# Kernel optimization log

Measured on AMD Instinct MI355X. Metric: run time of the kernel, lower is better.

## Reference

```python
import jax, jax.numpy as jnp
import numpy as np

B, L, D_MODEL = 2, 2048, 512
EXPAND = 2
ED = EXPAND * D_MODEL          # d_inner = 1024
N = 16                          # d_state
D_CONV = 4
DT_RANK = (D_MODEL + N - 1) // N  # 32
D_FF = 1024
EPS = 1e-5


def _mamba_params(key, pre):
    ks = jax.random.split(key, 6)
    s = 0.02
    p = {}
    p[pre + 'in_w'] = jax.random.normal(ks[0], (D_MODEL, 2 * ED), jnp.float32) * s
    p[pre + 'conv_w'] = jax.random.normal(ks[1], (ED, 1, D_CONV), jnp.float32) * s
    p[pre + 'conv_b'] = jnp.zeros((ED,), jnp.float32)
    p[pre + 'xproj_w'] = jax.random.normal(ks[2], (ED, DT_RANK + 2 * N), jnp.float32) * s
    p[pre + 'dt_w'] = jax.random.normal(ks[3], (DT_RANK, ED), jnp.float32) * s
    p[pre + 'dt_b'] = jax.random.normal(ks[4], (ED,), jnp.float32) * s
    # S4D-real init: A_log = log(1..N) per channel
    p[pre + 'A_log'] = jnp.log(jnp.broadcast_to(jnp.arange(1, N + 1, dtype=jnp.float32), (ED, N)))
    p[pre + 'D'] = jnp.ones((ED,), jnp.float32)
    p[pre + 'out_w'] = jax.random.normal(ks[5], (ED, D_MODEL), jnp.float32) * s
    return p


def setup_inputs() -> dict:
    key = jax.random.key(0)
    k_x, k_f, k_b, k_ffn = jax.random.split(key, 4)
    inp = {'x': jax.random.normal(k_x, (B, L, D_MODEL), jnp.float32)}
    inp.update(_mamba_params(k_f, 'f_'))
    inp.update(_mamba_params(k_b, 'b_'))
    inp['norm1_g'] = jnp.ones((D_MODEL,), jnp.float32)
    inp['norm1_b'] = jnp.zeros((D_MODEL,), jnp.float32)
    inp['norm2_g'] = jnp.ones((D_MODEL,), jnp.float32)
    inp['norm2_b'] = jnp.zeros((D_MODEL,), jnp.float32)
    k1, k2 = jax.random.split(k_ffn)
    inp['ffn_w1'] = jax.random.normal(k1, (D_MODEL, D_FF), jnp.float32) * 0.02
    inp['ffn_b1'] = jnp.zeros((D_FF,), jnp.float32)
    inp['ffn_w2'] = jax.random.normal(k2, (D_FF, D_MODEL), jnp.float32) * 0.02
    inp['ffn_b2'] = jnp.zeros((D_MODEL,), jnp.float32)
    return inp


def _selective_scan(x, delta, A, Bm, C, Dp):
    # x, delta: (B,L,ED); A: (ED,N); Bm, C: (B,L,N); Dp: (ED,)
    def step(h, inp):
        x_t, d_t, B_t, C_t = inp  # (B,ED),(B,ED),(B,N),(B,N)
        dA = jnp.exp(d_t[..., None] * A)                      # (B,ED,N)
        dBx = (d_t * x_t)[..., None] * B_t[:, None, :]        # (B,ED,N)
        h = dA * h + dBx
        y = jnp.einsum('ben,bn->be', h, C_t)
        return h, y

    h0 = jnp.zeros((x.shape[0], ED, N), x.dtype)
    xs = (x.transpose(1, 0, 2), delta.transpose(1, 0, 2),
          Bm.transpose(1, 0, 2), C.transpose(1, 0, 2))
    _, ys = jax.lax.scan(step, h0, xs)
    return ys.transpose(1, 0, 2) + x * Dp


def _mamba(x, in_w, conv_w, conv_b, xproj_w, dt_w, dt_b, A_log, Dp, out_w):
    xz = x @ in_w                                  # (B,L,2*ED)
    xs, z = jnp.split(xz, 2, axis=-1)
    # depthwise causal conv over time
    xc = jax.lax.conv_general_dilated(
        xs.transpose(0, 2, 1), conv_w, (1,), [(D_CONV - 1, 0)],
        dimension_numbers=('NCH', 'OIH', 'NCH'), feature_group_count=ED)
    xc = jax.nn.silu(xc.transpose(0, 2, 1) + conv_b)          # (B,L,ED)
    dbl = xc @ xproj_w                                        # (B,L,DT_RANK+2N)
    dt = dbl[..., :DT_RANK]
    Bm = dbl[..., DT_RANK:DT_RANK + N]
    C = dbl[..., DT_RANK + N:]
    delta = jax.nn.softplus(dt @ dt_w + dt_b)                 # (B,L,ED)
    A = -jnp.exp(A_log)
    y = _selective_scan(xc, delta, A, Bm, C, Dp)
    y = y * jax.nn.silu(z)
    return y @ out_w


def _layernorm(h, g, b):
    mu = jnp.mean(h, axis=-1, keepdims=True)
    var = jnp.var(h, axis=-1, keepdims=True)
    return (h - mu) * jax.lax.rsqrt(var + EPS) * g + b


def _ffn(h, w1, b1, w2, b2):
    return jnp.maximum(h @ w1 + b1, 0.0) @ w2 + b2


def reference(x,
              f_in_w, f_conv_w, f_conv_b, f_xproj_w, f_dt_w, f_dt_b, f_A_log, f_D, f_out_w,
              b_in_w, b_conv_w, b_conv_b, b_xproj_w, b_dt_w, b_dt_b, b_A_log, b_D, b_out_w,
              norm1_g, norm1_b, norm2_g, norm2_b,
              ffn_w1, ffn_b1, ffn_w2, ffn_b2):
    mf = _mamba(x, f_in_w, f_conv_w, f_conv_b, f_xproj_w, f_dt_w, f_dt_b, f_A_log, f_D, f_out_w)
    mf = _layernorm(mf, norm1_g, norm1_b)
    out_f = _ffn(mf, ffn_w1, ffn_b1, ffn_w2, ffn_b2) + mf
    # NOTE: original code computes norm2 but then uses the UN-normalized
    # backward output (variable shadowing bug); we replicate that faithfully.
    mb = _mamba(jnp.flip(x, axis=1), b_in_w, b_conv_w, b_conv_b, b_xproj_w,
                b_dt_w, b_dt_b, b_A_log, b_D, b_out_w)
    out_b = _ffn(mb, ffn_w1, ffn_b1, ffn_w2, ffn_b2) + mb
    return out_f + out_b
```

## Files before the change

### kernel.cpp

```cpp
#include <hip/hip_runtime.h>
#include <hip/hip_bf16.h>
#include <math.h>


#define BD 2
#define LD 2048
#define DMODEL 512
#define EDIM 1024
#define NST 16
#define DTR 32
#define DFF 1024
#define MROWS (BD*LD)

typedef __hip_bfloat16 bf16;
typedef __bf16 bf16x8 __attribute__((ext_vector_type(8)));
typedef float  f32x4  __attribute__((ext_vector_type(4)));

__device__ __forceinline__ float sig_(float x) { return 1.f / (1.f + __expf(-x)); }

__global__ __launch_bounds__(256)
void prep_k(const float* __restrict__ x, bf16* __restrict__ xbf,
            const float* __restrict__ inw_f, const float* __restrict__ inw_b,
            bf16* __restrict__ inwT,
            const float* __restrict__ outw_f, const float* __restrict__ outw_b,
            bf16* __restrict__ outwT,
            const float* __restrict__ fw1, bf16* __restrict__ fw1T,
            const float* __restrict__ fw2, bf16* __restrict__ fw2T)
{
    const int bid = blockIdx.x, tid = threadIdx.x;
    if (bid < 2048) {
        size_t i = (size_t)bid * 1024 + tid * 4;
        float4 v = *(const float4*)(x + i);
        bf16* o = xbf + i;
        o[0] = __float2bfloat16(v.x); o[1] = __float2bfloat16(v.y);
        o[2] = __float2bfloat16(v.z); o[3] = __float2bfloat16(v.w);
        return;
    }
    const float* W; bf16* WT; int R, C, cx, ry;
    if (bid < 4096) {
        int d = (bid - 2048) >> 10, t = (bid - 2048) & 1023;
        W = d ? inw_b : inw_f; WT = inwT + (size_t)d * 2048 * 512;
        R = 512; C = 2048; cx = t & 63; ry = t >> 6;
    } else if (bid < 5120) {
        int d = (bid - 4096) >> 9, t = (bid - 4096) & 511;
        W = d ? outw_b : outw_f; WT = outwT + (size_t)d * 512 * 1024;
        R = 1024; C = 512; cx = t & 15; ry = t >> 4;
    } else if (bid < 5632) {
        int t = bid - 5120; W = fw1; WT = fw1T; R = 512; C = 1024;
        cx = t & 31; ry = t >> 5;
    } else {
        int t = bid - 5632; W = fw2; WT = fw2T; R = 1024; C = 512;
        cx = t & 15; ry = t >> 4;
    }
    __shared__ float tt[32][33];
    const int c0 = cx * 32, r0 = ry * 32;
    const int col = tid & 31, rr = tid >> 5;
#pragma unroll
    for (int p = 0; p < 4; ++p)
        tt[p * 8 + rr][col] = W[(size_t)(r0 + p * 8 + rr) * C + c0 + col];
    __syncthreads();
#pragma unroll
    for (int p = 0; p < 4; ++p)
        WT[(size_t)(c0 + p * 8 + rr) * R + r0 + col] =
            __float2bfloat16(tt[col][p * 8 + rr]);
}

template<int BM, int BN, int MODE, bool FLIPD1>
__global__ __launch_bounds__(256)
void bgemm2_k(const bf16* __restrict__ A, size_t Astr, int lda,
              const bf16* __restrict__ BT, size_t Bstr,
              const float* __restrict__ bias,
              bf16* __restrict__ Cb, size_t Cstr, int ldc,
              const bf16* __restrict__ mp, size_t mpStr,
              float* __restrict__ outp,
              int M, int N, int K, int zoff)
{
    constexpr int FRm = BM / 32, FRn = BN / 32;
    __shared__ __align__(16) bf16 As[BM][40];
    __shared__ __align__(16) bf16 Bs[BN][40];
    const int tid = threadIdx.x;
    const int dir = blockIdx.z + zoff;
    const bool flip = FLIPD1 && (dir == 1);
    const bf16* Ad = A + (size_t)dir * Astr;
    const bf16* Bd = BT + (size_t)dir * Bstr;
    bf16* Cd = Cb ? Cb + (size_t)dir * Cstr : nullptr;
    const bf16* mpd = mp ? mp + (size_t)dir * mpStr : nullptr;
    const int bm = blockIdx.y * BM, bn = blockIdx.x * BN;
    const int wave = tid >> 6, lane = tid & 63;
    const int wm = (wave >> 1) * (BM / 2), wn = (wave & 1) * (BN / 2);
    const int lm = lane & 15, lq = lane >> 4;
    f32x4 acc[FRm][FRn] = {};

    for (int k0 = 0; k0 < K; k0 += 32) {
#pragma unroll
        for (int p = 0; p < BM / 64; ++p) {
            int row = p * 64 + (tid >> 2), col = (tid & 3) * 8;
            int gm = bm + row;
            if (flip) gm = (gm & ~(LD - 1)) + (LD - 1 - (gm & (LD - 1)));
            *(bf16x8*)&As[row][col] =
                *(const bf16x8*)(Ad + (size_t)gm * lda + k0 + col);
        }
#pragma unroll
        for (int p = 0; p < BN / 64; ++p) {
            int row = p * 64 + (tid >> 2), col = (tid & 3) * 8;
            *(bf16x8*)&Bs[row][col] =
                *(const bf16x8*)(Bd + (size_t)(bn + row) * K + k0 + col);
        }
        __syncthreads();

        bf16x8 af[FRm], bfr[FRn];
#pragma unroll
        for (int i = 0; i < FRm; ++i)
            af[i] = *(const bf16x8*)&As[wm + 16 * i + lm][lq * 8];
#pragma unroll
        for (int j = 0; j < FRn; ++j)
            bfr[j] = *(const bf16x8*)&Bs[wn + 16 * j + lm][lq * 8];
#pragma unroll
        for (int i = 0; i < FRm; ++i)
#pragma unroll
            for (int j = 0; j < FRn; ++j)
                acc[i][j] = __builtin_amdgcn_mfma_f32_16x16x32_bf16(
                    af[i], bfr[j], acc[i][j], 0, 0, 0);
        __syncthreads();
    }

#pragma unroll
    for (int i = 0; i < FRm; ++i) {
#pragma unroll
        for (int j = 0; j < FRn; ++j) {
            int col = bn + wn + 16 * j + lm;
            float bv = (MODE >= 2) ? bias[col] : 0.f;
#pragma unroll
            for (int r = 0; r < 4; ++r) {
                int row = bm + wm + 16 * i + lq * 4 + r;
                float v = acc[i][j][r] + bv;
                size_t idx = (size_t)row * ldc + col;
                if (MODE == 0)      Cd[idx] = __float2bfloat16(v);
                else if (MODE == 2) Cd[idx] = __float2bfloat16(fmaxf(v, 0.f));
                else if (MODE == 3) outp[idx] = v + __bfloat162float(mpd[idx]);
                else                outp[idx] += v + __bfloat162float(mpd[idx]);
            }
        }
    }
}

__global__ __launch_bounds__(256)
void zgate_k(const bf16* __restrict__ xbf, const bf16* __restrict__ inwT,
             const bf16* __restrict__ y2t_all, bf16* __restrict__ yrow_all)
{
    __shared__ __align__(16) bf16 As[64][40];
    __shared__ __align__(16) bf16 Bs[128][40];
    __shared__ __bf16 sy[64][130];
    const int tid = threadIdx.x;
    const int dir = blockIdx.z;
    const bf16* Bd = inwT + (size_t)dir * (2048 * 512) + (size_t)1024 * 512;
    const bf16* y2t = y2t_all + (size_t)dir * ((size_t)MROWS * EDIM);
    bf16* yrow = yrow_all + (size_t)dir * ((size_t)MROWS * EDIM);
    const int bm = blockIdx.y * 64, bn = blockIdx.x * 128;
    const int wave = tid >> 6, lane = tid & 63;
    const int wm = (wave >> 1) * 32, wn = (wave & 1) * 64;
    const int lm = lane & 15, lq = lane >> 4;
    f32x4 acc[2][4] = {};

    for (int k0 = 0; k0 < 512; k0 += 32) {
        {
            int row = tid >> 2, col = (tid & 3) * 8;
            int gm = bm + row;
            if (dir == 1) gm = (gm & ~(LD - 1)) + (LD - 1 - (gm & (LD - 1)));
            *(bf16x8*)&As[row][col] =
                *(const bf16x8*)(xbf + (size_t)gm * 512 + k0 + col);
        }
#pragma unroll
        for (int p = 0; p < 2; ++p) {
            int row = p * 64 + (tid >> 2), col = (tid & 3) * 8;
            *(bf16x8*)&Bs[row][col] =
                *(const bf16x8*)(Bd + (size_t)(bn + row) * 512 + k0 + col);
        }
        __syncthreads();
        bf16x8 af[2], bfr[4];
#pragma unroll
        for (int i = 0; i < 2; ++i)
            af[i] = *(const bf16x8*)&As[wm + 16 * i + lm][lq * 8];
#pragma unroll
        for (int j = 0; j < 4; ++j)
            bfr[j] = *(const bf16x8*)&Bs[wn + 16 * j + lm][lq * 8];
#pragma unroll
        for (int i = 0; i < 2; ++i)
#pragma unroll
            for (int j = 0; j < 4; ++j)
                acc[i][j] = __builtin_amdgcn_mfma_f32_16x16x32_bf16(
                    af[i], bfr[j], acc[i][j], 0, 0, 0);
        __syncthreads();
    }

    {
        const int b = bm >> 11, l0 = bm & (LD - 1);
        int e = tid >> 1, lh = (tid & 1) * 32;
        const bf16* yp = y2t + ((size_t)b * EDIM + bn + e) * LD + l0 + lh;
#pragma unroll
        for (int i = 0; i < 4; ++i) {
            bf16x8 v = *(const bf16x8*)(yp + i * 8);
#pragma unroll
            for (int j = 0; j < 8; ++j) sy[lh + i * 8 + j][e] = v[j];
        }
    }
    __syncthreads();
#pragma unroll
    for (int i = 0; i < 2; ++i) {
#pragma unroll
        for (int j = 0; j < 4; ++j) {
            int col = bn + wn + 16 * j + lm;
#pragma unroll
            for (int r = 0; r < 4; ++r) {
                int row = bm + wm + 16 * i + lq * 4 + r;
                float z = acc[i][j][r];
                float g = z * sig_(z);
                float y = (float)sy[(row - bm)][col - bn];
                yrow[(size_t)row * EDIM + col] = __float2bfloat16(g * y);
            }
        }
    }
}

__global__ __launch_bounds__(256)
void conv2_k(const bf16* __restrict__ xs2,
             const float* __restrict__ cw_f, const float* __restrict__ cb_f,
             const float* __restrict__ cw_b, const float* __restrict__ cb_b,
             bf16* __restrict__ xct2)
{
    __shared__ float sxs[67][64];
    __shared__ float sout[64][65];
    const int tid = threadIdx.x;
    const int dir = blockIdx.z;
    const bf16* xs = xs2 + (size_t)dir * ((size_t)MROWS * EDIM);
    const float* w  = dir ? cw_b : cw_f;
    const float* cb = dir ? cb_b : cb_f;
    bf16* xct = xct2 + (size_t)dir * ((size_t)MROWS * EDIM);
    const int e0 = blockIdx.x * 64;
    const int bl0 = blockIdx.y * 64;
    const int lloc0 = bl0 & (LD - 1);
    const int b = bl0 >> 11;
    {
        int row4 = tid >> 6, col = tid & 63;
#pragma unroll
        for (int i = 0; i < 17; ++i) {
            int hr = i * 4 + row4;
            if (hr < 67) {
                int lr = lloc0 + hr - 3;
                sxs[hr][col] = (lr >= 0)
                    ? __bfloat162float(xs[(size_t)(bl0 + hr - 3) * EDIM + e0 + col]) : 0.f;
            }
        }
    }
    __syncthreads();
    {
        int lr4 = tid >> 6, e = tid & 63;
        float w0 = w[(e0 + e) * 4 + 0], w1 = w[(e0 + e) * 4 + 1];
        float w2 = w[(e0 + e) * 4 + 2], w3 = w[(e0 + e) * 4 + 3];
        float cbv = cb[e0 + e];
#pragma unroll
        for (int i = 0; i < 16; ++i) {
            int lr = i * 4 + lr4;
            float acc = cbv;
            acc = fmaf(sxs[lr + 0][e], w0, acc);
            acc = fmaf(sxs[lr + 1][e], w1, acc);
            acc = fmaf(sxs[lr + 2][e], w2, acc);
            acc = fmaf(sxs[lr + 3][e], w3, acc);
            sout[e][lr] = acc * sig_(acc);
        }
    }
    __syncthreads();
    {
        int er4 = tid >> 6, l = tid & 63;
#pragma unroll
        for (int i = 0; i < 16; ++i) {
            int er = i * 4 + er4;
            xct[((size_t)b * EDIM + e0 + er) * LD + lloc0 + l] =
                __float2bfloat16(sout[er][l]);
        }
    }
}

__global__ __launch_bounds__(256)
void g2_k(const bf16* __restrict__ xct2, const float* __restrict__ xp_f,
          const float* __restrict__ xp_b, float* __restrict__ dblt2)
{
    __shared__ __align__(16) float As[32][18];
    __shared__ __align__(16) float Bs[32][66];
    const int tid = threadIdx.x;
    const int dir = blockIdx.y;
    const bf16* xct = xct2 + (size_t)dir * ((size_t)MROWS * EDIM);
    const float* xproj = dir ? xp_b : xp_f;
    float* dblt = dblt2 + (size_t)dir * (2 * 64 * LD);
    const int r0 = blockIdx.x * 16;
    const int bB = r0 >> 11, l0 = r0 & (LD - 1);
    const int row = tid >> 4, col4 = (tid & 15) * 4;
    float acc[4] = {};

    for (int k0 = 0; k0 < EDIM; k0 += 32) {
        {
            int k = tid >> 3, ls = (tid & 7) * 2;
            const bf16* p = xct + ((size_t)bB * EDIM + k0 + k) * LD + l0 + ls;
            As[k][ls] = __bfloat162float(p[0]);
            As[k][ls + 1] = __bfloat162float(p[1]);
        }
        {
            int k = tid >> 3, ns = (tid & 7) * 8;
            const float* p = xproj + (size_t)(k0 + k) * 64 + ns;
            float4 v0 = *(const float4*)p, v1 = *(const float4*)(p + 4);
            float* d = &Bs[k][ns];
            d[0]=v0.x; d[1]=v0.y; d[2]=v0.z; d[3]=v0.w;
            d[4]=v1.x; d[5]=v1.y; d[6]=v1.z; d[7]=v1.w;
        }
        __syncthreads();
#pragma unroll
        for (int kk = 0; kk < 32; ++kk) {
            float a = As[kk][row];
            float4 b4 = *(const float4*)&Bs[kk][col4];
            acc[0] = fmaf(a, b4.x, acc[0]);
            acc[1] = fmaf(a, b4.y, acc[1]);
            acc[2] = fmaf(a, b4.z, acc[2]);
            acc[3] = fmaf(a, b4.w, acc[3]);
        }
        __syncthreads();
    }
#pragma unroll
    for (int j = 0; j < 4; ++j)
        dblt[((size_t)bB * 64 + col4 + j) * LD + l0 + row] = acc[j];
}

__global__ __launch_bounds__(256)
void g3_k(const float* __restrict__ dblt2,
          const float* __restrict__ dtw_f, const float* __restrict__ dtb_f,
          const float* __restrict__ dtw_b, const float* __restrict__ dtb_b,
          bf16* __restrict__ dltt2)
{
    __shared__ __align__(16) float As[16][68];
    __shared__ __align__(16) float Bs[16][68];
    const int tid = threadIdx.x;
    const int dir = blockIdx.z;
    const float* Ap = dblt2 + (size_t)dir * (2 * 64 * LD);
    const float* Bw = dir ? dtw_b : dtw_f;
    const float* bias = dir ? dtb_b : dtb_f;
    bf16* Ct = dltt2 + (size_t)dir * ((size_t)MROWS * EDIM);
    const int bm = blockIdx.y * 64;
    const int bn = blockIdx.x * 64;
    const int bB = bm >> 11, l0 = bm & (LD - 1);
    const int tx = tid & 15, ty = tid >> 4;
    float acc[4][4] = {};

    for (int k0 = 0; k0 < DTR; k0 += 16) {
#pragma unroll
        for (int i = 0; i < 4; ++i) {
            int k = i * 4 + (tid >> 6), ll = tid & 63;
            As[k][ll] = Ap[((size_t)bB * 64 + k0 + k) * LD + l0 + ll];
        }
#pragma unroll
        for (int i = 0; i < 4; ++i) {
            int idx = tid + 256 * i;
            int nl = idx & 63, kl = idx >> 6;
            Bs[kl][nl] = Bw[(size_t)(k0 + kl) * EDIM + bn + nl];
        }
        __syncthreads();
#pragma unroll
        for (int kk = 0; kk < 16; ++kk) {
            float4 av = *(const float4*)&As[kk][ty * 4];
            float4 bv = *(const float4*)&Bs[kk][tx * 4];
            float a[4] = {av.x, av.y, av.z, av.w};
            float b[4] = {bv.x, bv.y, bv.z, bv.w};
#pragma unroll
            for (int i = 0; i < 4; ++i)
#pragma unroll
                for (int j = 0; j < 4; ++j)
                    acc[i][j] = fmaf(a[i], b[j], acc[i][j]);
        }
        __syncthreads();
    }
#pragma unroll
    for (int i = 0; i < 4; ++i) {
        int r = bm + ty * 4 + i;
#pragma unroll
        for (int j = 0; j < 4; ++j) {
            int c = bn + tx * 4 + j;
            float v = acc[i][j] + bias[c];
            v = (v > 20.f) ? v : log1pf(__expf(v));
            Ct[((size_t)(r >> 11) * EDIM + c) * LD + (r & (LD - 1))] =
                __float2bfloat16(v);
        }
    }
}

__global__ __launch_bounds__(256)
void scan6_k(bf16* __restrict__ xct2, const bf16* __restrict__ dltt2,
             const float* __restrict__ dblt2,
             const float* __restrict__ alog_f, const float* __restrict__ alog_b,
             const float* __restrict__ dp_f, const float* __restrict__ dp_b)
{
    __shared__ float sA[NST];
    __shared__ float sWp[NST][4];
    __shared__ float sWs[NST][4];
    const int gid = blockIdx.x;
    const int dir = gid >> 11;
    const int bb  = (gid >> 10) & 1;
    const int e   = gid & (EDIM - 1);
    const float* A_log = dir ? alog_b : alog_f;
    const float* Dp    = dir ? dp_b   : dp_f;
    bf16* xct = xct2 + (size_t)dir * ((size_t)MROWS * EDIM);
    const bf16* dltt = dltt2 + (size_t)dir * ((size_t)MROWS * EDIM);
    const float* bt = dblt2 + (size_t)dir * (2 * 64 * LD) + (size_t)bb * 64 * LD;
    const int tid = threadIdx.x;
    const int wave = tid >> 6, lane = tid & 63;
    const size_t baset = ((size_t)bb * EDIM + e) * LD;
    const int l0 = tid * 8;

    if (tid < NST) sA[tid] = -__expf(A_log[e * NST + tid]);

    float xv[8], dv[8], dx[8];
    {
        bf16x8 xr = *(const bf16x8*)(xct + baset + l0);
        bf16x8 dr = *(const bf16x8*)(dltt + baset + l0);
#pragma unroll
        for (int j = 0; j < 8; ++j) { xv[j] = (float)xr[j]; dv[j] = (float)dr[j]; }
    }
#pragma unroll
    for (int j = 0; j < 8; ++j) dx[j] = dv[j] * xv[j];
    __syncthreads();

    float y[8] = {};
    for (int n = 0; n < NST; ++n) {
        const float An = sA[n];
        const float* Bp = bt + (size_t)(DTR + n) * LD + l0;
        const float* Cp = bt + (size_t)(DTR + NST + n) * LD + l0;
        float4 b0 = *(const float4*)Bp, b1 = *(const float4*)(Bp + 4);
        float4 c0 = *(const float4*)Cp, c1 = *(const float4*)(Cp + 4);
        float Br[8] = {b0.x,b0.y,b0.z,b0.w, b1.x,b1.y,b1.z,b1.w};
        float Cr[8] = {c0.x,c0.y,c0.z,c0.w, c1.x,c1.y,c1.z,c1.w};

        float S[8], P[8];
        float h = 0.f, pr = 1.f;
#pragma unroll
        for (int l = 0; l < 8; ++l) {
            float a = __expf(dv[l] * An);
            pr *= a;
            h = fmaf(a, h, dx[l] * Br[l]);
            P[l] = pr; S[l] = h;
        }

        float p = pr, s = h;
#pragma unroll
        for (int d = 1; d < 64; d <<= 1) {
            float pp = __shfl_up(p, d, 64);
            float sp = __shfl_up(s, d, 64);
            if (lane >= d) { s = fmaf(sp, p, s); p *= pp; }
        }
        if (lane == 63) { sWp[n][wave] = p; sWs[n][wave] = s; }
        __syncthreads();
        float Hoff = 0.f;
#pragma unroll
        for (int w = 0; w < 3; ++w)
            if (w < wave) Hoff = fmaf(sWp[n][w], Hoff, sWs[n][w]);
        float pprev = __shfl_up(p, 1, 64);
        float sprev = __shfl_up(s, 1, 64);
        float H = (lane == 0) ? Hoff : fmaf(pprev, Hoff, sprev);

#pragma unroll
        for (int l = 0; l < 8; ++l)
            y[l] = fmaf(Cr[l], fmaf(P[l], H, S[l]), y[l]);
    }

    const float Dv = Dp[e];
    bf16x8 o;
#pragma unroll
    for (int l = 0; l < 8; ++l) o[l] = (__bf16)fmaf(xv[l], Dv, y[l]);
    *(bf16x8*)(xct + baset + l0) = o;
}

__global__ __launch_bounds__(256)
void ln_k(bf16* __restrict__ m, const float* __restrict__ gg,
          const float* __restrict__ bb)
{
    int row = (blockIdx.x * 256 + threadIdx.x) >> 6;
    int lane = threadIdx.x & 63;
    bf16* r = m + (size_t)row * DMODEL;
    float v[8], s = 0.f, s2 = 0.f;
#pragma unroll
    for (int i = 0; i < 8; ++i) {
        v[i] = __bfloat162float(r[lane + 64 * i]);
        s += v[i]; s2 = fmaf(v[i], v[i], s2);
    }
#pragma unroll
    for (int off = 32; off >= 1; off >>= 1) {
        s  += __shfl_xor(s, off, 64);
        s2 += __shfl_xor(s2, off, 64);
    }
    float mu = s * (1.f / DMODEL);
    float var = s2 * (1.f / DMODEL) - mu * mu;
    float inv = rsqrtf(var + 1e-5f);
#pragma unroll
    for (int i = 0; i < 8; ++i)
        r[lane + 64 * i] = __float2bfloat16(
            (v[i] - mu) * inv * gg[lane + 64 * i] + bb[lane + 64 * i]);
}

__global__ void sentinel_k(float* __restrict__ o)
{
    int i = blockIdx.x * 256 + threadIdx.x;
    o[i] = 100.0f;
}

extern "C" void kernel_launch(void* const* d_in, const int* in_sizes, int n_in,
                              void* d_out, int out_size, void* d_ws, size_t ws_size,
                              hipStream_t stream)
{
    const float* x    = (const float*)d_in[0];
    const float* n1g  = (const float*)d_in[19];
    const float* n1b  = (const float*)d_in[20];
    const float* fw1  = (const float*)d_in[23];
    const float* fb1  = (const float*)d_in[24];
    const float* fw2  = (const float*)d_in[25];
    const float* fb2  = (const float*)d_in[26];
    float* out = (float*)d_out;

    const size_t MiB = 1024 * 1024;
    const size_t SZ_DM = (size_t)MROWS * DMODEL;
    if (ws_size < 46 * MiB) {
        sentinel_k<<<dim3(SZ_DM / 256), dim3(256), 0, stream>>>(out);
        return;
    }

    char* base = (char*)d_ws;
    bf16* fw1T  = (bf16*)base;
    bf16* fw2T  = (bf16*)(base + 1 * MiB);
    bf16* outwT = (bf16*)(base + 2 * MiB);
    bf16* inwT  = (bf16*)(base + 4 * MiB);
    bf16* xbf   = (bf16*)(base + 8 * MiB);
    char* RA    = base + 12 * MiB;
    bf16* xs2   = (bf16*)RA;
    bf16* dltt2 = (bf16*)RA;
    bf16* yrow2 = (bf16*)RA;
    bf16* ffh2  = (bf16*)RA;
    char* RB    = base + 28 * MiB;
    bf16* xct2  = (bf16*)RB;
    bf16* mbf2  = (bf16*)RB;
    float* dblt2 = (float*)(base + 44 * MiB);

    const float* inw_f  = (const float*)d_in[1];
    const float* cw_f   = (const float*)d_in[2];
    const float* cb_f   = (const float*)d_in[3];
    const float* xp_f   = (const float*)d_in[4];
    const float* dtw_f  = (const float*)d_in[5];
    const float* dtb_f  = (const float*)d_in[6];
    const float* alog_f = (const float*)d_in[7];
    const float* dp_f   = (const float*)d_in[8];
    const float* outw_f = (const float*)d_in[9];
    const float* inw_b  = (const float*)d_in[10];
    const float* cw_b   = (const float*)d_in[11];
    const float* cb_b   = (const float*)d_in[12];
    const float* xp_b   = (const float*)d_in[13];
    const float* dtw_b  = (const float*)d_in[14];
    const float* dtb_b  = (const float*)d_in[15];
    const float* alog_b = (const float*)d_in[16];
    const float* dp_b   = (const float*)d_in[17];
    const float* outw_b = (const float*)d_in[18];

    dim3 blk(256);
    const size_t U = (size_t)MROWS * EDIM;

    prep_k<<<dim3(6144), blk, 0, stream>>>(x, xbf, inw_f, inw_b, inwT,
                                           outw_f, outw_b, outwT,
                                           fw1, fw1T, fw2, fw2T);
    bgemm2_k<64, 128, 0, true><<<dim3(8, 64, 2), blk, 0, stream>>>(
        xbf, 0, DMODEL, inwT, (size_t)2048 * 512, nullptr,
        xs2, U, EDIM, nullptr, 0, nullptr, MROWS, EDIM, DMODEL, 0);
    conv2_k<<<dim3(16, 64, 2), blk, 0, stream>>>(xs2, cw_f, cb_f, cw_b, cb_b, xct2);
    g2_k<<<dim3(256, 2), blk, 0, stream>>>(xct2, xp_f, xp_b, dblt2);
    g3_k<<<dim3(16, 64, 2), blk, 0, stream>>>(dblt2, dtw_f, dtb_f, dtw_b, dtb_b, dltt2);
    scan6_k<<<dim3(4096), blk, 0, stream>>>(xct2, dltt2, dblt2,
                                            alog_f, alog_b, dp_f, dp_b);
    zgate_k<<<dim3(8, 64, 2), blk, 0, stream>>>(xbf, inwT, xct2, yrow2);
    bgemm2_k<64, 64, 0, false><<<dim3(8, 64, 2), blk, 0, stream>>>(
        yrow2, U, EDIM, outwT, (size_t)512 * 1024, nullptr,
        mbf2, SZ_DM, DMODEL, nullptr, 0, nullptr, MROWS, DMODEL, EDIM, 0);
    ln_k<<<dim3(MROWS / 4), blk, 0, stream>>>(mbf2, n1g, n1b);
    bgemm2_k<64, 128, 2, false><<<dim3(8, 64, 2), blk, 0, stream>>>(
        mbf2, SZ_DM, DMODEL, fw1T, 0, fb1,
        ffh2, U, DFF, nullptr, 0, nullptr, MROWS, DFF, DMODEL, 0);
    bgemm2_k<64, 64, 3, false><<<dim3(8, 64, 1), blk, 0, stream>>>(
        ffh2, U, DFF, fw2T, 0, fb2,
        nullptr, 0, DMODEL, mbf2, SZ_DM, out, MROWS, DMODEL, DFF, 0);
    bgemm2_k<64, 64, 4, false><<<dim3(8, 64, 1), blk, 0, stream>>>(
        ffh2, U, DFF, fw2T, 0, fb2,
        nullptr, 0, DMODEL, mbf2, SZ_DM, out, MROWS, DMODEL, DFF, 1);
}
```

Measured before the change: 426.9 us.

## Use direct global-to-LDS loads, larger GEMM tiles, merged FFN2 and faster scan exps

GEMM staging now uses global_load_lds builtins with unpadded 128-row tiles. The two FFN second-layer GEMMs (forward and backward) become one GEMM that concatenates along K, with a doubled bias and the sum of both residuals, removing a read-modify-write pass over the output. The scan now checks at runtime whether A is linear in n and, if so, replaces the per-state exps with repeated multiplication. The trade-offs are unpadded LDS rows that may cause bank conflicts, fewer blocks per GEMM, and an exp fast path that only applies when A has this linear structure.

```diff
diff --git a/kernel.cpp b/kernel.cpp
--- a/kernel.cpp
+++ b/kernel.cpp
@@ -17,6 +17,13 @@
 typedef float  f32x4  __attribute__((ext_vector_type(4)));
 
 __device__ __forceinline__ float sig_(float x) { return 1.f / (1.f + __expf(-x)); }
+
+__device__ __forceinline__ void glds16(const void* g, void* l)
+{
+    __builtin_amdgcn_global_load_lds(
+        (const __attribute__((address_space(1))) void*)g,
+        (__attribute__((address_space(3))) void*)l, 16, 0, 0);
+}
 
 __global__ __launch_bounds__(256)
 void prep_k(const float* __restrict__ x, bf16* __restrict__ xbf,
@@ -65,46 +72,50 @@
             __float2bfloat16(tt[col][p * 8 + rr]);
 }
 
-template<int BM, int BN, int MODE, bool FLIPD1>
-__global__ __launch_bounds__(256)
-void bgemm2_k(const bf16* __restrict__ A, size_t Astr, int lda,
-              const bf16* __restrict__ BT, size_t Bstr,
+template<int BN, int MODE, bool FLIPD1, bool CATK>
+__global__ __launch_bounds__(256)
+void bgemm3_k(const bf16* __restrict__ A, size_t Astr, int lda,
+              const bf16* __restrict__ BT, size_t Bstr, int ldb,
               const float* __restrict__ bias,
               bf16* __restrict__ Cb, size_t Cstr, int ldc,
               const bf16* __restrict__ mp, size_t mpStr,
-              float* __restrict__ outp,
-              int M, int N, int K, int zoff)
-{
-    constexpr int FRm = BM / 32, FRn = BN / 32;
-    __shared__ __align__(16) bf16 As[BM][40];
-    __shared__ __align__(16) bf16 Bs[BN][40];
+              float* __restrict__ outp, int K)
+{
+    constexpr int BM = 128;
+    constexpr int FRm = 4, FRn = BN / 32;
+    constexpr int KH = DFF;
+    __shared__ __align__(16) bf16 As[BM][32];
+    __shared__ __align__(16) bf16 Bs[BN][32];
     const int tid = threadIdx.x;
-    const int dir = blockIdx.z + zoff;
+    const int dir = blockIdx.z;
     const bool flip = FLIPD1 && (dir == 1);
-    const bf16* Ad = A + (size_t)dir * Astr;
+    const bf16* Ad = A + (CATK ? (size_t)0 : (size_t)dir * Astr);
     const bf16* Bd = BT + (size_t)dir * Bstr;
-    bf16* Cd = Cb ? Cb + (size_t)dir * Cstr : nullptr;
-    const bf16* mpd = mp ? mp + (size_t)dir * mpStr : nullptr;
     const int bm = blockIdx.y * BM, bn = blockIdx.x * BN;
     const int wave = tid >> 6, lane = tid & 63;
-    const int wm = (wave >> 1) * (BM / 2), wn = (wave & 1) * (BN / 2);
+    const int wm = (wave >> 1) * 64, wn = (wave & 1) * (BN / 2);
     const int lm = lane & 15, lq = lane >> 4;
+    const int lrow = lane >> 2, lcol = (lane & 3) * 8;
     f32x4 acc[FRm][FRn] = {};
 
     for (int k0 = 0; k0 < K; k0 += 32) {
-#pragma unroll
-        for (int p = 0; p < BM / 64; ++p) {
-            int row = p * 64 + (tid >> 2), col = (tid & 3) * 8;
+        const bf16* Ab = Ad;
+        int ka = k0;
+        if (CATK && k0 >= KH) { Ab = A + Astr; ka = k0 - KH; }
+        const int kb = CATK ? (k0 & (KH - 1)) : k0;
+#pragma unroll
+        for (int c = 0; c < 2; ++c) {
+            int row = c * 64 + wave * 16 + lrow;
             int gm = bm + row;
             if (flip) gm = (gm & ~(LD - 1)) + (LD - 1 - (gm & (LD - 1)));
-            *(bf16x8*)&As[row][col] =
-                *(const bf16x8*)(Ad + (size_t)gm * lda + k0 + col);
-        }
-#pragma unroll
-        for (int p = 0; p < BN / 64; ++p) {
-            int row = p * 64 + (tid >> 2), col = (tid & 3) * 8;
-            *(bf16x8*)&Bs[row][col] =
-                *(const bf16x8*)(Bd + (size_t)(bn + row) * K + k0 + col);
+            glds16(Ab + (size_t)gm * lda + ka + lcol,
+                   &As[c * 64 + wave * 16][0]);
+        }
+#pragma unroll
+        for (int c = 0; c < BN / 64; ++c) {
+            int row = c * 64 + wave * 16 + lrow;
+            glds16(Bd + (size_t)(bn + row) * ldb + kb + lcol,
+                   &Bs[c * 64 + wave * 16][0]);
         }
         __syncthreads();
 
@@ -124,12 +135,14 @@
         __syncthreads();
     }
 
+    bf16* Cd = (MODE == 5) ? nullptr : Cb + (size_t)dir * Cstr;
 #pragma unroll
     for (int i = 0; i < FRm; ++i) {
 #pragma unroll
         for (int j = 0; j < FRn; ++j) {
             int col = bn + wn + 16 * j + lm;
-            float bv = (MODE >= 2) ? bias[col] : 0.f;
+            float bv = (MODE == 2) ? bias[col]
+                     : (MODE == 5) ? 2.f * bias[col] : 0.f;
 #pragma unroll
             for (int r = 0; r < 4; ++r) {
                 int row = bm + wm + 16 * i + lq * 4 + r;
@@ -137,8 +150,11 @@
                 size_t idx = (size_t)row * ldc + col;
                 if (MODE == 0)      Cd[idx] = __float2bfloat16(v);
                 else if (MODE == 2) Cd[idx] = __float2bfloat16(fmaxf(v, 0.f));
-                else if (MODE == 3) outp[idx] = v + __bfloat162float(mpd[idx]);
-                else                outp[idx] += v + __bfloat162float(mpd[idx]);
+                else {
+                    float m2 = __bfloat162float(mp[idx])
+                             + __bfloat162float(mp[mpStr + idx]);
+                    outp[idx] = v + m2;
+                }
             }
         }
     }
@@ -391,7 +407,7 @@
 }
 
 __global__ __launch_bounds__(256)
-void scan6_k(bf16* __restrict__ xct2, const bf16* __restrict__ dltt2,
+void scan7_k(bf16* __restrict__ xct2, const bf16* __restrict__ dltt2,
              const float* __restrict__ dblt2,
              const float* __restrict__ alog_f, const float* __restrict__ alog_b,
              const float* __restrict__ dp_f, const float* __restrict__ dp_b)
@@ -426,6 +442,21 @@
     for (int j = 0; j < 8; ++j) dx[j] = dv[j] * xv[j];
     __syncthreads();
 
+    bool linA = true;
+    {
+        float A1 = sA[0];
+#pragma unroll
+        for (int n = 1; n < NST; ++n)
+            linA = linA && (fabsf(sA[n] - A1 * (float)(n + 1))
+                            <= 1e-4f * (float)(n + 1));
+    }
+    float q[8], dA[8];
+    if (linA) {
+        float A1 = sA[0];
+#pragma unroll
+        for (int l = 0; l < 8; ++l) { q[l] = __expf(A1 * dv[l]); dA[l] = q[l]; }
+    }
+
     float y[8] = {};
     for (int n = 0; n < NST; ++n) {
         const float An = sA[n];
@@ -436,11 +467,16 @@
         float Br[8] = {b0.x,b0.y,b0.z,b0.w, b1.x,b1.y,b1.z,b1.w};
         float Cr[8] = {c0.x,c0.y,c0.z,c0.w, c1.x,c1.y,c1.z,c1.w};
 
+        if (!linA) {
+#pragma unroll
+            for (int l = 0; l < 8; ++l) dA[l] = __expf(dv[l] * An);
+        }
+
         float S[8], P[8];
         float h = 0.f, pr = 1.f;
 #pragma unroll
         for (int l = 0; l < 8; ++l) {
-            float a = __expf(dv[l] * An);
+            float a = dA[l];
             pr *= a;
             h = fmaf(a, h, dx[l] * Br[l]);
             P[l] = pr; S[l] = h;
@@ -466,6 +502,11 @@
 #pragma unroll
         for (int l = 0; l < 8; ++l)
             y[l] = fmaf(Cr[l], fmaf(P[l], H, S[l]), y[l]);
+
+        if (linA) {
+#pragma unroll
+            for (int l = 0; l < 8; ++l) dA[l] *= q[l];
+        }
     }
 
     const float Dv = Dp[e];
@@ -569,26 +610,23 @@
     prep_k<<<dim3(6144), blk, 0, stream>>>(x, xbf, inw_f, inw_b, inwT,
                                            outw_f, outw_b, outwT,
                                            fw1, fw1T, fw2, fw2T);
-    bgemm2_k<64, 128, 0, true><<<dim3(8, 64, 2), blk, 0, stream>>>(
-        xbf, 0, DMODEL, inwT, (size_t)2048 * 512, nullptr,
-        xs2, U, EDIM, nullptr, 0, nullptr, MROWS, EDIM, DMODEL, 0);
+    bgemm3_k<128, 0, true, false><<<dim3(8, 32, 2), blk, 0, stream>>>(
+        xbf, 0, DMODEL, inwT, (size_t)2048 * 512, DMODEL, nullptr,
+        xs2, U, EDIM, nullptr, 0, nullptr, DMODEL);
     conv2_k<<<dim3(16, 64, 2), blk, 0, stream>>>(xs2, cw_f, cb_f, cw_b, cb_b, xct2);
     g2_k<<<dim3(256, 2), blk, 0, stream>>>(xct2, xp_f, xp_b, dblt2);
     g3_k<<<dim3(16, 64, 2), blk, 0, stream>>>(dblt2, dtw_f, dtb_f, dtw_b, dtb_b, dltt2);
-    scan6_k<<<dim3(4096), blk, 0, stream>>>(xct2, dltt2, dblt2,
+    scan7_k<<<dim3(4096), blk, 0, stream>>>(xct2, dltt2, dblt2,
                                             alog_f, alog_b, dp_f, dp_b);
     zgate_k<<<dim3(8, 64, 2), blk, 0, stream>>>(xbf, inwT, xct2, yrow2);
-    bgemm2_k<64, 64, 0, false><<<dim3(8, 64, 2), blk, 0, stream>>>(
-        yrow2, U, EDIM, outwT, (size_t)512 * 1024, nullptr,
-        mbf2, SZ_DM, DMODEL, nullptr, 0, nullptr, MROWS, DMODEL, EDIM, 0);
+    bgemm3_k<64, 0, false, false><<<dim3(8, 32, 2), blk, 0, stream>>>(
+        yrow2, U, EDIM, outwT, (size_t)512 * 1024, EDIM, nullptr,
+        mbf2, SZ_DM, DMODEL, nullptr, 0, nullptr, EDIM);
     ln_k<<<dim3(MROWS / 4), blk, 0, stream>>>(mbf2, n1g, n1b);
-    bgemm2_k<64, 128, 2, false><<<dim3(8, 64, 2), blk, 0, stream>>>(
-        mbf2, SZ_DM, DMODEL, fw1T, 0, fb1,
-        ffh2, U, DFF, nullptr, 0, nullptr, MROWS, DFF, DMODEL, 0);
-    bgemm2_k<64, 64, 3, false><<<dim3(8, 64, 1), blk, 0, stream>>>(
-        ffh2, U, DFF, fw2T, 0, fb2,
-        nullptr, 0, DMODEL, mbf2, SZ_DM, out, MROWS, DMODEL, DFF, 0);
-    bgemm2_k<64, 64, 4, false><<<dim3(8, 64, 1), blk, 0, stream>>>(
-        ffh2, U, DFF, fw2T, 0, fb2,
-        nullptr, 0, DMODEL, mbf2, SZ_DM, out, MROWS, DMODEL, DFF, 1);
-}
+    bgemm3_k<128, 2, false, false><<<dim3(8, 32, 2), blk, 0, stream>>>(
+        mbf2, SZ_DM, DMODEL, fw1T, 0, DMODEL, fb1,
+        ffh2, U, DFF, nullptr, 0, nullptr, DMODEL);
+    bgemm3_k<64, 5, false, true><<<dim3(8, 32, 1), blk, 0, stream>>>(
+        ffh2, U, DFF, fw2T, 0, DFF, fb2,
+        nullptr, 0, DMODEL, mbf2, SZ_DM, out, 2 * DFF);
+}
```

Result: slower. 435.9 us (+2.1%).
